# Kernel optimization log

Hardware: AMD Instinct MI355X
Metric: run time of the kernel (lower is better)

The kernel has to match this reference:

```python
import jax, jax.numpy as jnp
import numpy as np

G = 4096              # number of graphs in batch
NPG = 198             # nodes per graph (fixed by view(-1, 198*2))
N = G * NPG           # total nodes = 811008
DEG = 8               # avg degree
E = N * DEG           # total edges = 6488064
CONV_DIMS = [(2, 20), (20, 15), (15, 10), (10, 5), (5, 2)]
MLP_DIMS = [(396, 200), (200, 100), (100, 50), (50, 10), (10, 2)]


def setup_inputs() -> dict:
    key = jax.random.key(0)
    ks = jax.random.split(key, 64)
    x = jax.random.normal(ks[0], (N, 2), dtype=jnp.float32)
    # block-diagonal edges: endpoints within each 198-node graph, then offset
    src = jax.random.randint(ks[1], (G, E // G), 0, NPG)
    dst = jax.random.randint(ks[2], (G, E // G), 0, NPG)
    off = (jnp.arange(G, dtype=jnp.int32) * NPG)[:, None]
    edge_index = jnp.stack([(src + off).reshape(-1), (dst + off).reshape(-1)]).astype(jnp.int32)
    edge_weight = jax.random.uniform(ks[3], (E,), dtype=jnp.float32)
    inp = {"x": x, "edge_index": edge_index, "edge_weight": edge_weight}
    ki = 4
    for i, (ci, co) in enumerate(CONV_DIMS):
        s = 1.0 / np.sqrt(ci)
        inp[f"w_rel{i}"] = jax.random.normal(ks[ki], (co, ci), jnp.float32) * s; ki += 1
        inp[f"b_rel{i}"] = jax.random.normal(ks[ki], (co,), jnp.float32) * s; ki += 1
        inp[f"w_root{i}"] = jax.random.normal(ks[ki], (co, ci), jnp.float32) * s; ki += 1
    for i, (ci, co) in enumerate(MLP_DIMS):
        s = 1.0 / np.sqrt(ci)
        inp[f"lw{i}"] = jax.random.normal(ks[ki], (co, ci), jnp.float32) * s; ki += 1
        inp[f"lb{i}"] = jax.random.normal(ks[ki], (co,), jnp.float32) * s; ki += 1
    return inp


def _graph_conv(x, src, dst, ew, w_rel, b_rel, w_root):
    # PyG GraphConv: lin_rel(sum_{j->i} e_ji * x_j) + lin_root(x_i)
    msg = x[src] * ew[:, None]                               # [E, Cin] gather
    agg = jax.ops.segment_sum(msg, dst, num_segments=N)      # [N, Cin] scatter-add
    return agg @ w_rel.T + b_rel + x @ w_root.T              # [N, Cout]


def reference(x, edge_index, edge_weight,
              w_rel0, b_rel0, w_root0, w_rel1, b_rel1, w_root1,
              w_rel2, b_rel2, w_root2, w_rel3, b_rel3, w_root3,
              w_rel4, b_rel4, w_root4,
              lw0, lb0, lw1, lb1, lw2, lb2, lw3, lb3, lw4, lb4):
    src, dst = edge_index[0], edge_index[1]
    convs = [(w_rel0, b_rel0, w_root0), (w_rel1, b_rel1, w_root1),
             (w_rel2, b_rel2, w_root2), (w_rel3, b_rel3, w_root3),
             (w_rel4, b_rel4, w_root4)]
    h = x
    for wr, br, wroot in convs:
        h = jax.nn.relu(_graph_conv(h, src, dst, edge_weight, wr, br, wroot))
    h = h.reshape(-1, NPG * 2)                               # [G, 396]
    mlp = [(lw0, lb0), (lw1, lb1), (lw2, lb2), (lw3, lb3)]
    for w, b in mlp:
        h = jax.nn.relu(h @ w.T + b)
    logits = h @ lw4.T + lb4                                 # [G, 2]
    return jax.nn.softmax(logits, axis=1)
```

## Files before the change

kernel.cpp:

```cpp
#include <hip/hip_runtime.h>
#include <hip/hip_fp16.h>

#define NG    4096
#define NPG   198
#define EPG   1584
#define ETOT  (NG * EPG)

#define BC2(u) __builtin_bit_cast(__half2, (u))

typedef _Float16 f16x4 __attribute__((ext_vector_type(4)));
typedef float    f32x4 __attribute__((ext_vector_type(4)));

#define H_F16S    (NG * 396)
#define WTB1_OFF  83200
#define WTB2_OFF  106496
#define WTB3_OFF  113664
#define WTB_TOTAL 114688

__global__ __launch_bounds__(256) void wtrans16_kernel(
    const float* __restrict__ w0, const float* __restrict__ w1,
    const float* __restrict__ w2, const float* __restrict__ w3,
    _Float16* __restrict__ wtb)
{
    const int idx = blockIdx.x * 256 + threadIdx.x;
    const float* w; int K, N, NPAD, rel;
    if (idx < 83200)       { w = w0; K = 396; N = 200; NPAD = 208; rel = idx; }
    else if (idx < 106496) { w = w1; K = 200; N = 100; NPAD = 112; rel = idx - 83200; }
    else if (idx < 113664) { w = w2; K = 100; N = 50;  NPAD = 64;  rel = idx - 106496; }
    else                   { w = w3; K = 50;  N = 10;  NPAD = 16;  rel = idx - 113664; }
    const int span = NPAD * 16;
    const int kc = rel / span;
    const int r  = rel - kc * span;
    const int n  = r >> 4, ki = r & 15;
    const int k  = kc * 16 + ki;
    const float v = (n < N && k < K) ? w[n * K + k] : 0.f;
    wtb[idx] = (_Float16)v;
}


template <int CIN, int COUT, int SIN, int SOUT>
__device__ __forceinline__ void conv_layer_h(
    const unsigned* __restrict__ h_in,
    unsigned* __restrict__ h_out,
    const unsigned* __restrict__ s_edge,
    const unsigned* __restrict__ row_start,
    const unsigned* __restrict__ perm,
    const float* __restrict__ wrel, const float* __restrict__ brel,
    const float* __restrict__ wroot, int tid)
{
    if (tid >= NPG) return;
    const int node = (int)perm[tid];
    constexpr int MS = (CIN + 1) / 2;

    __half2 ms[MS];
#pragma unroll
    for (int p = 0; p < MS; ++p) ms[p] = __floats2half2_rn(0.f, 0.f);

    const unsigned jb = row_start[node], je = row_start[node + 1];
    for (unsigned j = jb; j < je; ++j) {
        const unsigned e  = s_edge[j];
        const __half2  w2 = BC2((e >> 16) * 0x10001u);
        const unsigned* row = h_in + (e & 0xFFFFu) * SIN;
        if constexpr (SIN == 1) {
            ms[0] = __hfma2(w2, BC2(row[0]), ms[0]);
        } else {
            const uint4 q0 = *(const uint4*)row;
            ms[0] = __hfma2(w2, BC2(q0.x), ms[0]);
            if constexpr (MS > 1) ms[1] = __hfma2(w2, BC2(q0.y), ms[1]);
            if constexpr (MS > 2) ms[2] = __hfma2(w2, BC2(q0.z), ms[2]);
            if constexpr (MS > 3) ms[3] = __hfma2(w2, BC2(q0.w), ms[3]);
            if constexpr (MS > 4) {
                const uint4 q1 = *(const uint4*)(row + 4);
                ms[4] = __hfma2(w2, BC2(q1.x), ms[4]);
                if constexpr (MS > 5) ms[5] = __hfma2(w2, BC2(q1.y), ms[5]);
                if constexpr (MS > 6) ms[6] = __hfma2(w2, BC2(q1.z), ms[6]);
                if constexpr (MS > 7) ms[7] = __hfma2(w2, BC2(q1.w), ms[7]);
            }
            if constexpr (MS > 8) {
                const uint4 q2 = *(const uint4*)(row + 8);
                ms[8] = __hfma2(w2, BC2(q2.x), ms[8]);
                if constexpr (MS > 9) ms[9] = __hfma2(w2, BC2(q2.y), ms[9]);
            }
        }
    }

    float aggf[CIN];
#pragma unroll
    for (int p = 0; p < MS; ++p) {
        const float2 fa = __half22float2(ms[p]);
        aggf[2 * p] = fa.x;
        if (2 * p + 1 < CIN) aggf[2 * p + 1] = fa.y;
    }

    float hv[CIN];
    {
        const unsigned* me = h_in + node * SIN;
        unsigned mw[MS];
        if constexpr (SIN == 1) {
            mw[0] = me[0];
        } else {
            const uint4 q0 = *(const uint4*)me;
            mw[0] = q0.x;
            if constexpr (MS > 1) mw[1] = q0.y;
            if constexpr (MS > 2) mw[2] = q0.z;
            if constexpr (MS > 3) mw[3] = q0.w;
            if constexpr (MS > 4) {
                const uint4 q1 = *(const uint4*)(me + 4);
                mw[4] = q1.x;
                if constexpr (MS > 5) mw[5] = q1.y;
                if constexpr (MS > 6) mw[6] = q1.z;
                if constexpr (MS > 7) mw[7] = q1.w;
            }
            if constexpr (MS > 8) {
                const uint4 q2 = *(const uint4*)(me + 8);
                mw[8] = q2.x;
                if constexpr (MS > 9) mw[9] = q2.y;
            }
        }
#pragma unroll
        for (int p = 0; p < MS; ++p) {
            const float2 f = __half22float2(BC2(mw[p]));
            hv[2 * p] = f.x;
            if (2 * p + 1 < CIN) hv[2 * p + 1] = f.y;
        }
    }

    float outv[COUT];
#pragma unroll
    for (int o = 0; o < COUT; ++o) {
        float acc = brel[o];
#pragma unroll
        for (int c = 0; c < CIN; ++c) {
            acc = fmaf(aggf[c], wrel[o * CIN + c], acc);
            acc = fmaf(hv[c],   wroot[o * CIN + c], acc);
        }
        outv[o] = fmaxf(acc, 0.f);
    }

    if constexpr (SOUT == 1) {
        h_out[node] = __builtin_bit_cast(unsigned,
            __floats2half2_rn(outv[0], COUT > 1 ? outv[1] : 0.f));
    } else {
        constexpr int W  = (COUT + 1) / 2;
        constexpr int WQ = (W + 3) / 4;
        unsigned ow[WQ * 4];
#pragma unroll
        for (int p = 0; p < WQ * 4; ++p) {
            const float lo = (2 * p     < COUT) ? outv[2 * p]     : 0.f;
            const float hi = (2 * p + 1 < COUT) ? outv[2 * p + 1] : 0.f;
            ow[p] = __builtin_bit_cast(unsigned, __floats2half2_rn(lo, hi));
        }
        unsigned* orow = h_out + node * SOUT;
#pragma unroll
        for (int q = 0; q < WQ; ++q)
            *(uint4*)(orow + 4 * q) =
                make_uint4(ow[4*q], ow[4*q+1], ow[4*q+2], ow[4*q+3]);
    }
}

__global__ __launch_bounds__(256) void conv_kernel(
    const float* __restrict__ x,
    const int*   __restrict__ eidx,
    const float* __restrict__ ew,
    const float* wr0, const float* br0, const float* wq0,
    const float* wr1, const float* br1, const float* wq1,
    const float* wr2, const float* br2, const float* wq2,
    const float* wr3, const float* br3, const float* wq3,
    const float* wr4, const float* br4, const float* wq4,
    _Float16* __restrict__ H)
{
    __shared__ __align__(16) unsigned s_edge[EPG];
    __shared__ unsigned cnt[256];
    __shared__ unsigned cursor[256];
    __shared__ unsigned row_start[NPG + 1];
    __shared__ unsigned wsum[4];
    __shared__ unsigned dhist[64];
    __shared__ unsigned dcur[64];
    __shared__ unsigned perm[NPG];
    __shared__ __align__(16) unsigned bufA[NPG * 12];
    __shared__ __align__(16) unsigned bufB[NPG * 12];

    const int g = blockIdx.x, tid = threadIdx.x;
    const int ebase = g * EPG, nbase = g * NPG;
    const int lane = tid & 63, wid = tid >> 6;

    const int4*   s4 = (const int4*)(eidx + ebase);
    const int4*   d4 = (const int4*)(eidx + ETOT + ebase);
    const float4* w4 = (const float4*)(ew + ebase);
    const int4   sa = s4[tid];
    const int4   da = d4[tid];
    const float4 wa = w4[tid];
    const bool hasb = tid < (EPG / 4 - 256);
    int4 sb = {0,0,0,0}, db = {0,0,0,0}; float4 wb = {0,0,0,0};
    if (hasb) { sb = s4[tid + 256]; db = d4[tid + 256]; wb = w4[tid + 256]; }

    cnt[tid] = 0u;
    __syncthreads();
    atomicAdd(&cnt[da.x - nbase], 1u); atomicAdd(&cnt[da.y - nbase], 1u);
    atomicAdd(&cnt[da.z - nbase], 1u); atomicAdd(&cnt[da.w - nbase], 1u);
    if (hasb) {
        atomicAdd(&cnt[db.x - nbase], 1u); atomicAdd(&cnt[db.y - nbase], 1u);
        atomicAdd(&cnt[db.z - nbase], 1u); atomicAdd(&cnt[db.w - nbase], 1u);
    }
    __syncthreads();

    const unsigned v = cnt[tid];
    unsigned inc = v;
#pragma unroll
    for (int s = 1; s < 64; s <<= 1) {
        const unsigned t = (unsigned)__shfl_up((int)inc, s);
        if (lane >= s) inc += t;
    }
    if (lane == 63) wsum[wid] = inc;
    __syncthreads();
    unsigned pre = 0;
    for (int w = 0; w < wid; ++w) pre += wsum[w];
    const unsigned excl = pre + inc - v;
    if (tid <= NPG) row_start[tid] = excl;
    if (tid < NPG)  cursor[tid]    = excl;
    __syncthreads();

    {
        auto place = [&](int s, int d, float w) {
            const int dl = d - nbase;
            const unsigned slot = atomicAdd(&cursor[dl], 1u);
            const __half hw = __float2half_rn(w);
            s_edge[slot] = ((unsigned)__half_as_ushort(hw) << 16)
                         | (unsigned)(s - nbase);
        };
        place(sa.x, da.x, wa.x); place(sa.y, da.y, wa.y);
        place(sa.z, da.z, wa.z); place(sa.w, da.w, wa.w);
        if (hasb) {
            place(sb.x, db.x, wb.x); place(sb.y, db.y, wb.y);
            place(sb.z, db.z, wb.z); place(sb.w, db.w, wb.w);
        }
    }

    if (tid < NPG) {
        const float2 xv = ((const float2*)x)[nbase + tid];
        bufA[tid] = __builtin_bit_cast(unsigned, __floats2half2_rn(xv.x, xv.y));
    }

    if (tid < 64) dhist[tid] = 0u;
    __syncthreads();
    unsigned mydeg = 0u;
    if (tid < NPG) {
        mydeg = cnt[tid]; if (mydeg > 63u) mydeg = 63u;
        atomicAdd(&dhist[mydeg], 1u);
    }
    __syncthreads();
    if (tid < 64) {
        const unsigned dv = dhist[tid];
        unsigned sc = dv;
#pragma unroll
        for (int s = 1; s < 64; s <<= 1) {
            const unsigned t = (unsigned)__shfl_up((int)sc, s);
            if (lane >= s) sc += t;
        }
        dcur[tid] = sc - dv;
    }
    __syncthreads();
    if (tid < NPG) {
        const unsigned pos = atomicAdd(&dcur[mydeg], 1u);
        perm[pos] = (unsigned)tid;
    }
    __syncthreads();

    conv_layer_h<2,  20, 1,  12>(bufA, bufB, s_edge, row_start, perm, wr0, br0, wq0, tid);
    __syncthreads();
    conv_layer_h<20, 15, 12, 12>(bufB, bufA, s_edge, row_start, perm, wr1, br1, wq1, tid);
    __syncthreads();
    conv_layer_h<15, 10, 12, 12>(bufA, bufB, s_edge, row_start, perm, wr2, br2, wq2, tid);
    __syncthreads();
    conv_layer_h<10, 5,  12, 12>(bufB, bufA, s_edge, row_start, perm, wr3, br3, wq3, tid);
    __syncthreads();
    conv_layer_h<5,  2,  12, 1 >(bufA, bufB, s_edge, row_start, perm, wr4, br4, wq4, tid);
    __syncthreads();

    if (tid < NPG)
        ((unsigned*)H)[g * 198 + tid] = bufB[tid];
}


__device__ __forceinline__ void zero_words(void* p, int nwords, int tid)
{
    unsigned* u = (unsigned*)p;
    for (int i = tid; i < nwords; i += 256) u[i] = 0u;
}

template<int KC, int NTT, int NOUT, int SIN, int SOUT>
__device__ __forceinline__ void mfma_layer(
    const _Float16* __restrict__ inb,
    _Float16* __restrict__ outb,
    const _Float16* __restrict__ wtb,
    const float* __restrict__ bias, int tid)
{
    constexpr int NPAD = NTT * 16;
    const int lane = tid & 63, wid = tid >> 6;
    const int lrow = lane & 15, lgrp = lane >> 4;
    const _Float16* aptr = inb + lrow * SIN + lgrp * 4;

    for (int nt0 = wid; nt0 < NTT; nt0 += 8) {
        const int  nt1  = nt0 + 4;
        const bool has2 = nt1 < NTT;
        f32x4 acc0 = {0.f, 0.f, 0.f, 0.f};
        f32x4 acc1 = {0.f, 0.f, 0.f, 0.f};
        const int n0 = nt0 * 16 + lrow;
        const int n1 = nt1 * 16 + lrow;
        const _Float16* b0 = wtb + n0 * 16 + lgrp * 4;
        const _Float16* b1 = wtb + n1 * 16 + lgrp * 4;
#pragma unroll 4
        for (int kc = 0; kc < KC; ++kc) {
            const f16x4 a   = *(const f16x4*)(aptr + kc * 16);
            const f16x4 vb0 = *(const f16x4*)(b0 + (size_t)kc * (NPAD * 16));
            acc0 = __builtin_amdgcn_mfma_f32_16x16x16f16(a, vb0, acc0, 0, 0, 0);
            if (has2) {
                const f16x4 vb1 = *(const f16x4*)(b1 + (size_t)kc * (NPAD * 16));
                acc1 = __builtin_amdgcn_mfma_f32_16x16x16f16(a, vb1, acc1, 0, 0, 0);
            }
        }
        if (n0 < NOUT) {
            const float bv = bias[n0];
#pragma unroll
            for (int j = 0; j < 4; ++j)
                outb[(lgrp * 4 + j) * SOUT + n0] =
                    (_Float16)fmaxf(acc0[j] + bv, 0.f);
        }
        if (has2 && n1 < NOUT) {
            const float bv = bias[n1];
#pragma unroll
            for (int j = 0; j < 4; ++j)
                outb[(lgrp * 4 + j) * SOUT + n1] =
                    (_Float16)fmaxf(acc1[j] + bv, 0.f);
        }
    }
}

__global__ __launch_bounds__(256) void mlp_mfma_kernel(
    const _Float16* __restrict__ H,
    const _Float16* __restrict__ wtb,
    const float* __restrict__ lb0, const float* __restrict__ lb1,
    const float* __restrict__ lb2, const float* __restrict__ lb3,
    const float* __restrict__ lw4, const float* __restrict__ lb4,
    float* __restrict__ out)
{
    __shared__ __align__(16) _Float16 bufH[16 * 400];
    __shared__ __align__(16) _Float16 bufX[16 * 224];
    __shared__ __align__(16) _Float16 bufY[16 * 128];

    const int tid   = threadIdx.x;
    const int gbase = blockIdx.x * 16;

    {
        const unsigned* Hw = (const unsigned*)H + (size_t)gbase * 198;
        unsigned* bH = (unsigned*)bufH;
        for (int t = tid; t < 16 * 200; t += 256) {
            const int gg = t / 200, w = t - gg * 200;
            bH[gg * 200 + w] = (w < 198) ? Hw[gg * 198 + w] : 0u;
        }
        zero_words(bufX, 16 * 224 / 2, tid);
        zero_words(bufY, 16 * 128 / 2, tid);
    }
    __syncthreads();

    mfma_layer<25, 13, 200, 400, 224>(bufH, bufX, wtb, lb0, tid);
    __syncthreads();

    zero_words(bufH, 512, tid);
    mfma_layer<13, 7, 100, 224, 128>(bufX, bufY, wtb + WTB1_OFF, lb1, tid);
    __syncthreads();

    zero_words(bufX, 128, tid);
    mfma_layer<7, 4, 50, 128, 64>(bufY, bufH, wtb + WTB2_OFF, lb2, tid);
    __syncthreads();

    mfma_layer<4, 1, 10, 64, 16>(bufH, bufX, wtb + WTB3_OFF, lb3, tid);
    __syncthreads();

    if (tid < 16) {
        float l0 = lb4[0], l1 = lb4[1];
#pragma unroll
        for (int k = 0; k < 10; ++k) {
            const float hv = (float)bufX[tid * 16 + k];
            l0 = fmaf(hv, lw4[k],      l0);
            l1 = fmaf(hv, lw4[10 + k], l1);
        }
        const float m  = fmaxf(l0, l1);
        const float e0 = __expf(l0 - m), e1 = __expf(l1 - m);
        const float inv = 1.f / (e0 + e1);
        float2 p; p.x = e0 * inv; p.y = e1 * inv;
        ((float2*)out)[gbase + tid] = p;
    }
}

extern "C" void kernel_launch(void* const* d_in, const int* in_sizes, int n_in,
                              void* d_out, int out_size, void* d_ws, size_t ws_size,
                              hipStream_t stream)
{
    const float* x    = (const float*)d_in[0];
    const int*   eidx = (const int*)  d_in[1];
    const float* ew   = (const float*)d_in[2];

    const float* wr[5]; const float* br[5]; const float* wq[5];
    for (int i = 0; i < 5; ++i) {
        wr[i] = (const float*)d_in[3 + 3 * i];
        br[i] = (const float*)d_in[4 + 3 * i];
        wq[i] = (const float*)d_in[5 + 3 * i];
    }
    const float* lw[5]; const float* lb[5];
    for (int i = 0; i < 5; ++i) {
        lw[i] = (const float*)d_in[18 + 2 * i];
        lb[i] = (const float*)d_in[19 + 2 * i];
    }

    _Float16* wsH = (_Float16*)d_ws;
    _Float16* wtb = wsH + (size_t)H_F16S;

    wtrans16_kernel<<<(WTB_TOTAL + 255) / 256, 256, 0, stream>>>(
        lw[0], lw[1], lw[2], lw[3], wtb);

    conv_kernel<<<NG, 256, 0, stream>>>(
        x, eidx, ew,
        wr[0], br[0], wq[0],
        wr[1], br[1], wq[1],
        wr[2], br[2], wq[2],
        wr[3], br[3], wq[3],
        wr[4], br[4], wq[4],
        wsH);

    mlp_mfma_kernel<<<NG / 16, 256, 0, stream>>>(
        wsH, wtb,
        lb[0], lb[1], lb[2], lb[3],
        lw[4], lb[4],
        (float*)d_out);
}
```

Baseline: 129.6 us.

## Use fp32 edge aggregation and split-fp16 MLP weights with 512-thread MLP blocks

The conv aggregation now accumulates in fp32 FMAs instead of packed half2 FMAs. The MLP weights are split into hi and lo fp16 parts, so each k-chunk issues twice as many MFMAs to recover precision close to fp32. The MLP kernel moves to 512 threads with one n-tile per wave, replacing the strided loop. These changes look aimed mainly at accuracy and add ALU and MFMA work, traded against a higher wave count in the MLP and zero-initialized shared buffers.

```diff
diff --git a/kernel.cpp b/kernel.cpp
--- a/kernel.cpp
+++ b/kernel.cpp
@@ -5,6 +5,7 @@
 #define NPG   198
 #define EPG   1584
 #define ETOT  (NG * EPG)
+#define SHW   12
 
 #define BC2(u) __builtin_bit_cast(__half2, (u))
 
@@ -12,10 +13,10 @@
 typedef float    f32x4 __attribute__((ext_vector_type(4)));
 
 #define H_F16S    (NG * 396)
+#define WTB_SZ    114688
 #define WTB1_OFF  83200
 #define WTB2_OFF  106496
 #define WTB3_OFF  113664
-#define WTB_TOTAL 114688
 
 __global__ __launch_bounds__(256) void wtrans16_kernel(
     const float* __restrict__ w0, const float* __restrict__ w1,
@@ -23,20 +24,23 @@
     _Float16* __restrict__ wtb)
 {
     const int idx = blockIdx.x * 256 + threadIdx.x;
+    if (idx >= 2 * WTB_SZ) return;
+    const int half = idx >= WTB_SZ;
+    const int rel0 = idx - half * WTB_SZ;
     const float* w; int K, N, NPAD, rel;
-    if (idx < 83200)       { w = w0; K = 396; N = 200; NPAD = 208; rel = idx; }
-    else if (idx < 106496) { w = w1; K = 200; N = 100; NPAD = 112; rel = idx - 83200; }
-    else if (idx < 113664) { w = w2; K = 100; N = 50;  NPAD = 64;  rel = idx - 106496; }
-    else                   { w = w3; K = 50;  N = 10;  NPAD = 16;  rel = idx - 113664; }
+    if (rel0 < 83200)       { w = w0; K = 396; N = 200; NPAD = 208; rel = rel0; }
+    else if (rel0 < 106496) { w = w1; K = 200; N = 100; NPAD = 112; rel = rel0 - 83200; }
+    else if (rel0 < 113664) { w = w2; K = 100; N = 50;  NPAD = 64;  rel = rel0 - 106496; }
+    else                    { w = w3; K = 50;  N = 10;  NPAD = 16;  rel = rel0 - 113664; }
     const int span = NPAD * 16;
     const int kc = rel / span;
     const int r  = rel - kc * span;
     const int n  = r >> 4, ki = r & 15;
     const int k  = kc * 16 + ki;
     const float v = (n < N && k < K) ? w[n * K + k] : 0.f;
-    wtb[idx] = (_Float16)v;
-}
-
+    const _Float16 hi = (_Float16)v;
+    wtb[idx] = half ? (_Float16)(v - (float)hi) : hi;
+}
 
 template <int CIN, int COUT, int SIN, int SOUT>
 __device__ __forceinline__ void conv_layer_h(
@@ -44,7 +48,7 @@
     unsigned* __restrict__ h_out,
     const unsigned* __restrict__ s_edge,
     const unsigned* __restrict__ row_start,
-    const unsigned* __restrict__ perm,
+    const unsigned short* __restrict__ perm,
     const float* __restrict__ wrel, const float* __restrict__ brel,
     const float* __restrict__ wroot, int tid)
 {
@@ -52,76 +56,53 @@
     const int node = (int)perm[tid];
     constexpr int MS = (CIN + 1) / 2;
 
-    __half2 ms[MS];
-#pragma unroll
-    for (int p = 0; p < MS; ++p) ms[p] = __floats2half2_rn(0.f, 0.f);
+    float aggf[MS * 2];
+#pragma unroll
+    for (int c = 0; c < MS * 2; ++c) aggf[c] = 0.f;
 
     const unsigned jb = row_start[node], je = row_start[node + 1];
     for (unsigned j = jb; j < je; ++j) {
         const unsigned e  = s_edge[j];
-        const __half2  w2 = BC2((e >> 16) * 0x10001u);
+        const float    wf = __half2float(__ushort_as_half((unsigned short)(e >> 16)));
         const unsigned* row = h_in + (e & 0xFFFFu) * SIN;
+        unsigned wv[MS];
         if constexpr (SIN == 1) {
-            ms[0] = __hfma2(w2, BC2(row[0]), ms[0]);
+            wv[0] = row[0];
         } else {
             const uint4 q0 = *(const uint4*)row;
-            ms[0] = __hfma2(w2, BC2(q0.x), ms[0]);
-            if constexpr (MS > 1) ms[1] = __hfma2(w2, BC2(q0.y), ms[1]);
-            if constexpr (MS > 2) ms[2] = __hfma2(w2, BC2(q0.z), ms[2]);
-            if constexpr (MS > 3) ms[3] = __hfma2(w2, BC2(q0.w), ms[3]);
+            wv[0] = q0.x;
+            if constexpr (MS > 1) wv[1] = q0.y;
+            if constexpr (MS > 2) wv[2] = q0.z;
+            if constexpr (MS > 3) wv[3] = q0.w;
             if constexpr (MS > 4) {
                 const uint4 q1 = *(const uint4*)(row + 4);
-                ms[4] = __hfma2(w2, BC2(q1.x), ms[4]);
-                if constexpr (MS > 5) ms[5] = __hfma2(w2, BC2(q1.y), ms[5]);
-                if constexpr (MS > 6) ms[6] = __hfma2(w2, BC2(q1.z), ms[6]);
-                if constexpr (MS > 7) ms[7] = __hfma2(w2, BC2(q1.w), ms[7]);
+                wv[4] = q1.x;
+                if constexpr (MS > 5) wv[5] = q1.y;
+                if constexpr (MS > 6) wv[6] = q1.z;
+                if constexpr (MS > 7) wv[7] = q1.w;
             }
             if constexpr (MS > 8) {
                 const uint4 q2 = *(const uint4*)(row + 8);
-                ms[8] = __hfma2(w2, BC2(q2.x), ms[8]);
-                if constexpr (MS > 9) ms[9] = __hfma2(w2, BC2(q2.y), ms[9]);
+                wv[8] = q2.x;
+                if constexpr (MS > 9) wv[9] = q2.y;
             }
         }
-    }
-
-    float aggf[CIN];
-#pragma unroll
-    for (int p = 0; p < MS; ++p) {
-        const float2 fa = __half22float2(ms[p]);
-        aggf[2 * p] = fa.x;
-        if (2 * p + 1 < CIN) aggf[2 * p + 1] = fa.y;
-    }
-
-    float hv[CIN];
+#pragma unroll
+        for (int p = 0; p < MS; ++p) {
+            const __half2 h2 = BC2(wv[p]);
+            aggf[2*p]     = fmaf(wf, __low2float(h2),  aggf[2*p]);
+            aggf[2*p + 1] = fmaf(wf, __high2float(h2), aggf[2*p + 1]);
+        }
+    }
+
+    float hv[MS * 2];
     {
         const unsigned* me = h_in + node * SIN;
-        unsigned mw[MS];
-        if constexpr (SIN == 1) {
-            mw[0] = me[0];
-        } else {
-            const uint4 q0 = *(const uint4*)me;
-            mw[0] = q0.x;
-            if constexpr (MS > 1) mw[1] = q0.y;
-            if constexpr (MS > 2) mw[2] = q0.z;
-            if constexpr (MS > 3) mw[3] = q0.w;
-            if constexpr (MS > 4) {
-                const uint4 q1 = *(const uint4*)(me + 4);
-                mw[4] = q1.x;
-                if constexpr (MS > 5) mw[5] = q1.y;
-                if constexpr (MS > 6) mw[6] = q1.z;
-                if constexpr (MS > 7) mw[7] = q1.w;
-            }
-            if constexpr (MS > 8) {
-                const uint4 q2 = *(const uint4*)(me + 8);
-                mw[8] = q2.x;
-                if constexpr (MS > 9) mw[9] = q2.y;
-            }
-        }
 #pragma unroll
         for (int p = 0; p < MS; ++p) {
-            const float2 f = __half22float2(BC2(mw[p]));
-            hv[2 * p] = f.x;
-            if (2 * p + 1 < CIN) hv[2 * p + 1] = f.y;
+            const __half2 h2 = BC2(me[p]);
+            hv[2*p]     = __low2float(h2);
+            hv[2*p + 1] = __high2float(h2);
         }
     }
 
@@ -141,20 +122,18 @@
         h_out[node] = __builtin_bit_cast(unsigned,
             __floats2half2_rn(outv[0], COUT > 1 ? outv[1] : 0.f));
     } else {
-        constexpr int W  = (COUT + 1) / 2;
-        constexpr int WQ = (W + 3) / 4;
-        unsigned ow[WQ * 4];
-#pragma unroll
-        for (int p = 0; p < WQ * 4; ++p) {
+        unsigned ow[SOUT];
+#pragma unroll
+        for (int p = 0; p < SOUT; ++p) {
             const float lo = (2 * p     < COUT) ? outv[2 * p]     : 0.f;
             const float hi = (2 * p + 1 < COUT) ? outv[2 * p + 1] : 0.f;
             ow[p] = __builtin_bit_cast(unsigned, __floats2half2_rn(lo, hi));
         }
         unsigned* orow = h_out + node * SOUT;
 #pragma unroll
-        for (int q = 0; q < WQ; ++q)
-            *(uint4*)(orow + 4 * q) =
-                make_uint4(ow[4*q], ow[4*q+1], ow[4*q+2], ow[4*q+3]);
+        for (int qn = 0; qn < SOUT / 4; ++qn)
+            *(uint4*)(orow + 4 * qn) =
+                make_uint4(ow[4*qn], ow[4*qn+1], ow[4*qn+2], ow[4*qn+3]);
     }
 }
 
@@ -170,19 +149,21 @@
     _Float16* __restrict__ H)
 {
     __shared__ __align__(16) unsigned s_edge[EPG];
-    __shared__ unsigned cnt[256];
-    __shared__ unsigned cursor[256];
-    __shared__ unsigned row_start[NPG + 1];
-    __shared__ unsigned wsum[4];
-    __shared__ unsigned dhist[64];
-    __shared__ unsigned dcur[64];
-    __shared__ unsigned perm[NPG];
-    __shared__ __align__(16) unsigned bufA[NPG * 12];
-    __shared__ __align__(16) unsigned bufB[NPG * 12];
+    __shared__ unsigned       cnt[256];
+    __shared__ unsigned       cursor[256];
+    __shared__ unsigned       row_start[NPG + 1];
+    __shared__ unsigned       wsum[4];
+    __shared__ unsigned       dhist[64];
+    __shared__ unsigned       dcur[64];
+    __shared__ unsigned short perm[NPG + 2];
+    __shared__ __align__(16) unsigned bufA[NPG * SHW];
+    __shared__ __align__(16) unsigned bufB[NPG * SHW];
 
     const int g = blockIdx.x, tid = threadIdx.x;
     const int ebase = g * EPG, nbase = g * NPG;
     const int lane = tid & 63, wid = tid >> 6;
+
+    for (int i = tid; i < NPG * SHW; i += 256) { bufA[i] = 0u; bufB[i] = 0u; }
 
     const int4*   s4 = (const int4*)(eidx + ebase);
     const int4*   d4 = (const int4*)(eidx + ETOT + ebase);
@@ -245,7 +226,7 @@
     __syncthreads();
     unsigned mydeg = 0u;
     if (tid < NPG) {
-        mydeg = cnt[tid]; if (mydeg > 63u) mydeg = 63u;
+        mydeg = v; if (mydeg > 63u) mydeg = 63u;
         atomicAdd(&dhist[mydeg], 1u);
     }
     __syncthreads();
@@ -262,81 +243,83 @@
     __syncthreads();
     if (tid < NPG) {
         const unsigned pos = atomicAdd(&dcur[mydeg], 1u);
-        perm[pos] = (unsigned)tid;
-    }
-    __syncthreads();
-
-    conv_layer_h<2,  20, 1,  12>(bufA, bufB, s_edge, row_start, perm, wr0, br0, wq0, tid);
-    __syncthreads();
-    conv_layer_h<20, 15, 12, 12>(bufB, bufA, s_edge, row_start, perm, wr1, br1, wq1, tid);
-    __syncthreads();
-    conv_layer_h<15, 10, 12, 12>(bufA, bufB, s_edge, row_start, perm, wr2, br2, wq2, tid);
-    __syncthreads();
-    conv_layer_h<10, 5,  12, 12>(bufB, bufA, s_edge, row_start, perm, wr3, br3, wq3, tid);
-    __syncthreads();
-    conv_layer_h<5,  2,  12, 1 >(bufA, bufB, s_edge, row_start, perm, wr4, br4, wq4, tid);
+        perm[pos] = (unsigned short)tid;
+    }
+    __syncthreads();
+
+    conv_layer_h<2,  20, 1,   SHW>(bufA, bufB, s_edge, row_start, perm, wr0, br0, wq0, tid);
+    __syncthreads();
+    conv_layer_h<20, 15, SHW, SHW>(bufB, bufA, s_edge, row_start, perm, wr1, br1, wq1, tid);
+    __syncthreads();
+    conv_layer_h<15, 10, SHW, SHW>(bufA, bufB, s_edge, row_start, perm, wr2, br2, wq2, tid);
+    __syncthreads();
+    conv_layer_h<10, 5,  SHW, SHW>(bufB, bufA, s_edge, row_start, perm, wr3, br3, wq3, tid);
+    __syncthreads();
+    conv_layer_h<5,  2,  SHW, 1  >(bufA, bufB, s_edge, row_start, perm, wr4, br4, wq4, tid);
     __syncthreads();
 
     if (tid < NPG)
-        ((unsigned*)H)[g * 198 + tid] = bufB[tid];
-}
-
+        ((unsigned*)H)[g * NPG + tid] = bufB[tid];
+}
 
 __device__ __forceinline__ void zero_words(void* p, int nwords, int tid)
 {
     unsigned* u = (unsigned*)p;
-    for (int i = tid; i < nwords; i += 256) u[i] = 0u;
+    for (int i = tid; i < nwords; i += 512) u[i] = 0u;
 }
 
 template<int KC, int NTT, int NOUT, int SIN, int SOUT>
 __device__ __forceinline__ void mfma_layer(
     const _Float16* __restrict__ inb,
     _Float16* __restrict__ outb,
-    const _Float16* __restrict__ wtb,
+    const _Float16* __restrict__ wthi,
+    const _Float16* __restrict__ wtlo,
     const float* __restrict__ bias, int tid)
 {
     constexpr int NPAD = NTT * 16;
     const int lane = tid & 63, wid = tid >> 6;
     const int lrow = lane & 15, lgrp = lane >> 4;
+    const int nt0 = wid;
+    if (nt0 >= NTT) return;
+    const bool has2 = (nt0 + 8) < NTT;
     const _Float16* aptr = inb + lrow * SIN + lgrp * 4;
 
-    for (int nt0 = wid; nt0 < NTT; nt0 += 8) {
-        const int  nt1  = nt0 + 4;
-        const bool has2 = nt1 < NTT;
-        f32x4 acc0 = {0.f, 0.f, 0.f, 0.f};
-        f32x4 acc1 = {0.f, 0.f, 0.f, 0.f};
-        const int n0 = nt0 * 16 + lrow;
-        const int n1 = nt1 * 16 + lrow;
-        const _Float16* b0 = wtb + n0 * 16 + lgrp * 4;
-        const _Float16* b1 = wtb + n1 * 16 + lgrp * 4;
+    f32x4 acc0 = {0.f, 0.f, 0.f, 0.f};
+    f32x4 acc1 = {0.f, 0.f, 0.f, 0.f};
+    const int n0 = nt0 * 16 + lrow;
+    const int n1 = (nt0 + 8) * 16 + lrow;
+    const int boff0 = n0 * 16 + lgrp * 4;
+    const int boff1 = n1 * 16 + lgrp * 4;
 #pragma unroll 4
-        for (int kc = 0; kc < KC; ++kc) {
-            const f16x4 a   = *(const f16x4*)(aptr + kc * 16);
-            const f16x4 vb0 = *(const f16x4*)(b0 + (size_t)kc * (NPAD * 16));
-            acc0 = __builtin_amdgcn_mfma_f32_16x16x16f16(a, vb0, acc0, 0, 0, 0);
-            if (has2) {
-                const f16x4 vb1 = *(const f16x4*)(b1 + (size_t)kc * (NPAD * 16));
-                acc1 = __builtin_amdgcn_mfma_f32_16x16x16f16(a, vb1, acc1, 0, 0, 0);
-            }
-        }
-        if (n0 < NOUT) {
-            const float bv = bias[n0];
-#pragma unroll
-            for (int j = 0; j < 4; ++j)
-                outb[(lgrp * 4 + j) * SOUT + n0] =
-                    (_Float16)fmaxf(acc0[j] + bv, 0.f);
-        }
-        if (has2 && n1 < NOUT) {
-            const float bv = bias[n1];
-#pragma unroll
-            for (int j = 0; j < 4; ++j)
-                outb[(lgrp * 4 + j) * SOUT + n1] =
-                    (_Float16)fmaxf(acc1[j] + bv, 0.f);
-        }
-    }
-}
-
-__global__ __launch_bounds__(256) void mlp_mfma_kernel(
+    for (int kc = 0; kc < KC; ++kc) {
+        const f16x4 a = *(const f16x4*)(aptr + kc * 16);
+        const size_t kb = (size_t)kc * (NPAD * 16);
+        acc0 = __builtin_amdgcn_mfma_f32_16x16x16f16(
+            a, *(const f16x4*)(wthi + kb + boff0), acc0, 0, 0, 0);
+        acc0 = __builtin_amdgcn_mfma_f32_16x16x16f16(
+            a, *(const f16x4*)(wtlo + kb + boff0), acc0, 0, 0, 0);
+        if (has2) {
+            acc1 = __builtin_amdgcn_mfma_f32_16x16x16f16(
+                a, *(const f16x4*)(wthi + kb + boff1), acc1, 0, 0, 0);
+            acc1 = __builtin_amdgcn_mfma_f32_16x16x16f16(
+                a, *(const f16x4*)(wtlo + kb + boff1), acc1, 0, 0, 0);
+        }
+    }
+    if (n0 < NOUT) {
+        const float bv = bias[n0];
+#pragma unroll
+        for (int j = 0; j < 4; ++j)
+            outb[(lgrp * 4 + j) * SOUT + n0] = (_Float16)fmaxf(acc0[j] + bv, 0.f);
+    }
+    if (has2 && n1 < NOUT) {
+        const float bv = bias[n1];
+#pragma unroll
+        for (int j = 0; j < 4; ++j)
+            outb[(lgrp * 4 + j) * SOUT + n1] = (_Float16)fmaxf(acc1[j] + bv, 0.f);
+    }
+}
+
+__global__ __launch_bounds__(512) void mlp_mfma_kernel(
     const _Float16* __restrict__ H,
     const _Float16* __restrict__ wtb,
     const float* __restrict__ lb0, const float* __restrict__ lb1,
@@ -350,11 +333,12 @@
 
     const int tid   = threadIdx.x;
     const int gbase = blockIdx.x * 16;
+    const _Float16* lo = wtb + WTB_SZ;
 
     {
         const unsigned* Hw = (const unsigned*)H + (size_t)gbase * 198;
         unsigned* bH = (unsigned*)bufH;
-        for (int t = tid; t < 16 * 200; t += 256) {
+        for (int t = tid; t < 16 * 200; t += 512) {
             const int gg = t / 200, w = t - gg * 200;
             bH[gg * 200 + w] = (w < 198) ? Hw[gg * 198 + w] : 0u;
         }
@@ -363,18 +347,18 @@
     }
     __syncthreads();
 
-    mfma_layer<25, 13, 200, 400, 224>(bufH, bufX, wtb, lb0, tid);
+    mfma_layer<25, 13, 200, 400, 224>(bufH, bufX, wtb, lo, lb0, tid);
     __syncthreads();
 
     zero_words(bufH, 512, tid);
-    mfma_layer<13, 7, 100, 224, 128>(bufX, bufY, wtb + WTB1_OFF, lb1, tid);
+    mfma_layer<13, 7, 100, 224, 128>(bufX, bufY, wtb + WTB1_OFF, lo + WTB1_OFF, lb1, tid);
     __syncthreads();
 
     zero_words(bufX, 128, tid);
-    mfma_layer<7, 4, 50, 128, 64>(bufY, bufH, wtb + WTB2_OFF, lb2, tid);
-    __syncthreads();
-
-    mfma_layer<4, 1, 10, 64, 16>(bufH, bufX, wtb + WTB3_OFF, lb3, tid);
+    mfma_layer<7, 4, 50, 128, 64>(bufY, bufH, wtb + WTB2_OFF, lo + WTB2_OFF, lb2, tid);
+    __syncthreads();
+
+    mfma_layer<4, 1, 10, 64, 16>(bufH, bufX, wtb + WTB3_OFF, lo + WTB3_OFF, lb3, tid);
     __syncthreads();
 
     if (tid < 16) {
@@ -416,7 +400,7 @@
     _Float16* wsH = (_Float16*)d_ws;
     _Float16* wtb = wsH + (size_t)H_F16S;
 
-    wtrans16_kernel<<<(WTB_TOTAL + 255) / 256, 256, 0, stream>>>(
+    wtrans16_kernel<<<(2 * WTB_SZ + 255) / 256, 256, 0, stream>>>(
         lw[0], lw[1], lw[2], lw[3], wtb);
 
     conv_kernel<<<NG, 256, 0, stream>>>(
@@ -428,7 +412,7 @@
         wr[4], br[4], wq[4],
         wsH);
 
-    mlp_mfma_kernel<<<NG / 16, 256, 0, stream>>>(
+    mlp_mfma_kernel<<<NG / 16, 512, 0, stream>>>(
         wsH, wtb,
         lb[0], lb[1], lb[2], lb[3],
         lw[4], lb[4],
```

New measurement: 123.3 us. 4.8% less time.
